# Performance work log

Measured on AMD Instinct MI355X. Metric: run time of the kernel, lower is better.

## Reference

```python
import jax, jax.numpy as jnp
import numpy as np

N = 20000      # nodes / tokens
H = 256        # hidden_size
NH = 8         # num_heads
HD = NH * H    # num_heads * hidden_size = 2048
EPS = 1e-5


def setup_inputs() -> dict:
    key = jax.random.key(0)
    ks = jax.random.split(key, 24)

    def lin_w(k, i, o):
        # xavier-ish scale for a Linear weight stored as [in, out]
        return jax.random.normal(k, (i, o), jnp.float32) * (1.0 / np.sqrt(i))

    inp = {
        'q': jax.random.normal(ks[0], (N, H), jnp.float32),
        'k': jax.random.normal(ks[1], (N, H), jnp.float32),
        'v': jax.random.normal(ks[2], (N, H), jnp.float32),
        'layer': 1,
        'Wq1': lin_w(ks[3], H, HD), 'bq1': jnp.zeros((HD,), jnp.float32),
        'Wk1': lin_w(ks[4], H, HD), 'bk1': jnp.zeros((HD,), jnp.float32),
        'Wq2': lin_w(ks[5], H, HD), 'bq2': jnp.zeros((HD,), jnp.float32),
        'Wk2': lin_w(ks[6], H, HD), 'bk2': jnp.zeros((HD,), jnp.float32),
        'Wv':  lin_w(ks[7], H, HD), 'bv':  jnp.zeros((HD,), jnp.float32),
        'ln_g': jnp.ones((HD,), jnp.float32),
        'ln_b': jnp.zeros((HD,), jnp.float32),
        'Wo': lin_w(ks[8], HD, H), 'bo': jnp.zeros((H,), jnp.float32),
        'lq1': jax.random.normal(ks[9], (H,), jnp.float32) * 0.1,
        'lk1': jax.random.normal(ks[10], (H,), jnp.float32) * 0.1,
        'lq2': jax.random.normal(ks[11], (H,), jnp.float32) * 0.1,
        'lk2': jax.random.normal(ks[12], (H,), jnp.float32) * 0.1,
    }
    return inp


def reference(q, k, v, layer, Wq1, bq1, Wk1, bk1, Wq2, bq2, Wk2, bk2,
              Wv, bv, ln_g, ln_b, Wo, bo, lq1, lk1, lq2, lk2):
    # projections: [N, H] -> [N, HD]
    q1 = q @ Wq1 + bq1
    k1 = k @ Wk1 + bk1
    q2 = q @ Wq2 + bq2
    k2 = k @ Wk2 + bk2
    vv = v @ Wv + bv

    # linear attention: K^T V -> [HD, HD]  (dropout is identity in eval mode)
    k1v = k1.T @ vv
    k2v = k2.T @ vv

    # lambda gating (scalars)
    lam1 = jnp.exp(jnp.sum(lq1 * lk1))
    lam2 = jnp.exp(jnp.sum(lq2 * lk2))
    lam_init = 0.8 - 0.6 * jnp.exp(jnp.asarray(-0.3 * layer, jnp.float32))
    lam_full = lam1 - lam2 + lam_init

    # Q @ (K^T V), differential subtraction: [N, HD]
    x = q1 @ k1v - lam_full * (q2 @ k2v)

    # LayerNorm over last dim (biased variance, eps=1e-5, like torch)
    mu = jnp.mean(x, axis=-1, keepdims=True)
    var = jnp.mean(jnp.square(x - mu), axis=-1, keepdims=True)
    x = (x - mu) / jnp.sqrt(var + EPS) * ln_g + ln_b

    x = x * (1.0 - lam_init)
    return x @ Wo + bo  # [N, H]
```

## Files before the change

### kernel.cpp

```cpp
#include <hip/hip_runtime.h>
#include <stdint.h>

typedef __bf16 bf16x8 __attribute__((ext_vector_type(8)));
typedef float f32x4 __attribute__((ext_vector_type(4)));
typedef float f32x2 __attribute__((ext_vector_type(2)));
typedef unsigned short u16x4 __attribute__((ext_vector_type(4)));
typedef unsigned short u16x8 __attribute__((ext_vector_type(8)));

#define NTOK 20000
#define HIW  256
#define HD   2048
#define LDK  66
#define BUFS 8448

static __device__ __forceinline__ unsigned short f2bf(float f) {
  union { float f; unsigned u; } c; c.f = f;
  unsigned u = c.u + (0x7fffu + ((c.u >> 16) & 1u));
  return (unsigned short)(u >> 16);
}
static __device__ __forceinline__ float bf2f(unsigned short h) {
  union { unsigned u; float f; } c; c.u = ((unsigned)h) << 16;
  return c.f;
}

#define WRED(x) { x += __shfl_xor(x,32); x += __shfl_xor(x,16); x += __shfl_xor(x,8); \
                  x += __shfl_xor(x,4);  x += __shfl_xor(x,2);  x += __shfl_xor(x,1); }

__global__ __launch_bounds__(512) void k_front(
    const float* __restrict__ kk, const float* __restrict__ vv,
    const float* __restrict__ Wq1, const float* __restrict__ Wk1,
    const float* __restrict__ Wq2, const float* __restrict__ Wk2,
    const float* __restrict__ lq1, const float* __restrict__ lk1,
    const float* __restrict__ lq2, const float* __restrict__ lk2,
    const float* __restrict__ bq1, const float* __restrict__ bk1,
    const float* __restrict__ bq2, const float* __restrict__ bk2,
    const int* __restrict__ layer,
    float* __restrict__ S_part, float* __restrict__ skp, float* __restrict__ svp,
    float* __restrict__ Pc_part, float* __restrict__ scal) {
  __shared__ unsigned short SH[4 * BUFS];
  const int b = blockIdx.x;
  const int t = threadIdx.x, lane = t & 63, wave = t >> 6;
  const int wr = (wave >> 1) * 32, wc = (wave & 1) * 64;
  const int r15 = lane & 15, kg = (lane >> 4) * 8;

  if (b < 256) {
    const int z = b & 63, by = (b >> 6) & 1, bx = (b >> 7) & 1;
    const int i0 = bx * 128, j0 = by * 128;
    const int n_lo = z * 313;
    const int cnt = (NTOK - n_lo < 313) ? (NTOK - n_lo) : 313;
    f32x4 acc[2][4];
    #pragma unroll
    for (int m = 0; m < 2; ++m)
      #pragma unroll
      for (int n = 0; n < 4; ++n) acc[m][n] = (f32x4){0.f, 0.f, 0.f, 0.f};

    const int matsel = t >> 8, col = t & 127, half = (t >> 7) & 1;
    const float* src = matsel ? vv : kk;
    const int gcol = (matsel ? j0 : i0) + col;
    unsigned short* Lb0 = SH + matsel * BUFS;
    unsigned short* Lb1 = SH + 2 * BUFS + matsel * BUFS;
    const int tbase = half * 32;
    float csum = 0.f;
    float rA[32], rB[32];

#define LOADK(dst, KT)                                                        \
    { _Pragma("unroll")                                                       \
      for (int g = 0; g < 32; ++g) {                                          \
        int nn = (KT) * 64 + tbase + g;                                       \
        dst[g] = (nn < cnt) ? src[(size_t)(n_lo + nn) * HIW + gcol] : 0.f;    \
      } }
#define WRITEK(dstp, rr)                                                      \
    { _Pragma("unroll")                                                       \
      for (int g4 = 0; g4 < 8; ++g4) {                                        \
        u16x4 o;                                                              \
        _Pragma("unroll")                                                     \
        for (int u = 0; u < 4; ++u) {                                         \
          float x = rr[g4 * 4 + u]; csum += x; o[u] = f2bf(x);                \
        }                                                                     \
        *(u16x4*)&dstp[col * LDK + tbase + g4 * 4] = o;                       \
      } }

    LOADK(rA, 0)
    WRITEK(Lb0, rA)
    LOADK(rB, 1)
    asm volatile("s_waitcnt lgkmcnt(0)" ::: "memory");
    __builtin_amdgcn_s_barrier();

    #pragma unroll
    for (int kt = 0; kt < 5; ++kt) {
      const unsigned short* Akr = SH + (kt & 1) * 2 * BUFS;
      const unsigned short* Bkr = Akr + BUFS;
      #pragma unroll
      for (int ks = 0; ks < 2; ++ks) {
        const int ko = ks * 32 + kg;
        bf16x8 ah[2], bh[4];
        #pragma unroll
        for (int m = 0; m < 2; ++m)
          ah[m] = *(const bf16x8*)&Akr[(wr + m * 16 + r15) * LDK + ko];
        #pragma unroll
        for (int n = 0; n < 4; ++n)
          bh[n] = *(const bf16x8*)&Bkr[(wc + n * 16 + r15) * LDK + ko];
        #pragma unroll
        for (int m = 0; m < 2; ++m)
          #pragma unroll
          for (int n = 0; n < 4; ++n)
            acc[m][n] = __builtin_amdgcn_mfma_f32_16x16x32_bf16(ah[m], bh[n], acc[m][n], 0, 0, 0);
      }
      if (kt < 4) {
        unsigned short* Ld = SH + ((kt + 1) & 1) * 2 * BUFS + matsel * BUFS;
        if ((kt & 1) == 0) {
          WRITEK(Ld, rB)
          if (kt + 2 <= 4) LOADK(rA, kt + 2)
        } else {
          WRITEK(Ld, rA)
          if (kt + 2 <= 4) LOADK(rB, kt + 2)
        }
      }
      asm volatile("s_waitcnt lgkmcnt(0)" ::: "memory");
      __builtin_amdgcn_s_barrier();
    }
#undef LOADK
#undef WRITEK
    const int rg = (lane >> 4) * 4;
    #pragma unroll
    for (int m = 0; m < 2; ++m)
      #pragma unroll
      for (int n = 0; n < 4; ++n)
        #pragma unroll
        for (int r = 0; r < 4; ++r)
          S_part[(size_t)z * 65536 + (i0 + wr + m * 16 + rg + r) * 256 + (j0 + wc + n * 16 + r15)] =
              acc[m][n][r];
    if (bx == by) {
      float* red = (float*)SH;
      red[t] = csum;
      __syncthreads();
      if (t < 128)      skp[z * 256 + i0 + t]         = red[t] + red[t + 128];
      else if (t < 256) svp[z * 256 + j0 + (t - 128)] = red[t + 128] + red[t + 256];
    }
  } else if (b < 384) {
    const int idx = b - 256;
    const int pair = idx >> 6, rem = idx & 63;
    const int z = rem & 15, by = (rem >> 4) & 1, bx = (rem >> 5) & 1;
    const int i0 = bx * 128, j0 = by * 128;
    const float* Wa = pair ? Wq2 : Wq1;
    const float* Wb = pair ? Wk2 : Wk1;
    f32x4 acc[2][4];
    #pragma unroll
    for (int m = 0; m < 2; ++m)
      #pragma unroll
      for (int n = 0; n < 4; ++n) acc[m][n] = (f32x4){0.f, 0.f, 0.f, 0.f};
    unsigned short* Ak = SH;
    unsigned short* Bk = SH + BUFS;
    const int srow = t >> 2, sq = (t & 3) * 16;
    for (int kt = 0; kt < 2; ++kt) {
      const int kb = z * 128 + kt * 64 + sq;
      __syncthreads();
      #pragma unroll
      for (int c = 0; c < 4; ++c) {
        f32x4 a = *(const f32x4*)&Wa[(size_t)(i0 + srow) * HD + kb + c * 4];
        f32x4 bb = *(const f32x4*)&Wb[(size_t)(j0 + srow) * HD + kb + c * 4];
        u16x4 oa, ob;
        #pragma unroll
        for (int u = 0; u < 4; ++u) { oa[u] = f2bf(a[u]); ob[u] = f2bf(bb[u]); }
        *(u16x4*)&Ak[srow * LDK + sq + c * 4] = oa;
        *(u16x4*)&Bk[srow * LDK + sq + c * 4] = ob;
      }
      __syncthreads();
      #pragma unroll
      for (int ks = 0; ks < 2; ++ks) {
        const int ko = ks * 32 + kg;
        bf16x8 ah[2], bh[4];
        #pragma unroll
        for (int m = 0; m < 2; ++m)
          ah[m] = *(const bf16x8*)&Ak[(wr + m * 16 + r15) * LDK + ko];
        #pragma unroll
        for (int n = 0; n < 4; ++n)
          bh[n] = *(const bf16x8*)&Bk[(wc + n * 16 + r15) * LDK + ko];
        #pragma unroll
        for (int m = 0; m < 2; ++m)
          #pragma unroll
          for (int n = 0; n < 4; ++n)
            acc[m][n] = __builtin_amdgcn_mfma_f32_16x16x32_bf16(ah[m], bh[n], acc[m][n], 0, 0, 0);
      }
    }
    const int rg = (lane >> 4) * 4;
    #pragma unroll
    for (int m = 0; m < 2; ++m)
      #pragma unroll
      for (int n = 0; n < 4; ++n)
        #pragma unroll
        for (int r = 0; r < 4; ++r)
          Pc_part[(size_t)(pair * 16 + z) * 65536 +
                  (i0 + wr + m * 16 + rg + r) * 256 + (j0 + wc + n * 16 + r15)] = acc[m][n][r];
  } else {
    float* red = (float*)SH;
    if (t < 256) {
      float p1 = lq1[t] * lk1[t], p2 = lq2[t] * lk2[t];
      float d1 = 0.f, d2 = 0.f;
      #pragma unroll
      for (int u = 0; u < 8; ++u) {
        d1 += bq1[t * 8 + u] * bk1[t * 8 + u];
        d2 += bq2[t * 8 + u] * bk2[t * 8 + u];
      }
      WRED(p1); WRED(p2); WRED(d1); WRED(d2);
      int w = t >> 6;
      if ((t & 63) == 0) { red[w] = p1; red[4 + w] = p2; red[8 + w] = d1; red[12 + w] = d2; }
    }
    __syncthreads();
    if (t == 0) {
      float s1 = red[0] + red[1] + red[2] + red[3];
      float s2 = red[4] + red[5] + red[6] + red[7];
      float dd1 = red[8] + red[9] + red[10] + red[11];
      float dd2 = red[12] + red[13] + red[14] + red[15];
      float li = 0.8f - 0.6f * expf(-0.3f * (float)layer[0]);
      float lam = expf(s1) - expf(s2) + li;
      scal[0] = lam; scal[1] = -lam; scal[2] = 1.0f - li; scal[3] = li;
      scal[4] = dd1 - lam * dd2;
    }
  }
}

__global__ __launch_bounds__(256) void k_sred(
    const float* __restrict__ S_part, const float* __restrict__ Pc_part,
    const float* __restrict__ skp, const float* __restrict__ svp,
    float* __restrict__ S, float* __restrict__ Pc,
    float* __restrict__ sk, float* __restrict__ sv,
    const float* __restrict__ Wk1, const float* __restrict__ Wk2,
    const float* __restrict__ Wq1, const float* __restrict__ Wq2,
    const float* __restrict__ bq1, const float* __restrict__ bq2,
    const float* __restrict__ bk1, const float* __restrict__ bk2,
    const float* __restrict__ scal, float* __restrict__ gc, float* __restrict__ uc) {
  int b = blockIdx.x, t = threadIdx.x;
  if (b < 64) {
    size_t idx = (size_t)b * 1024 + t * 4;
    f32x4 s0 = {0.f, 0.f, 0.f, 0.f}, s1 = {0.f, 0.f, 0.f, 0.f};
    #pragma unroll 4
    for (int z = 0; z < 64; z += 2) {
      s0 += *(const f32x4*)&S_part[(size_t)z * 65536 + idx];
      s1 += *(const f32x4*)&S_part[(size_t)(z + 1) * 65536 + idx];
    }
    *(f32x4*)&S[idx] = s0 + s1;
  } else if (b < 128) {
    size_t idx = (size_t)(b - 64) * 1024 + t * 4;
    f32x4 s1 = {0.f, 0.f, 0.f, 0.f}, s2 = {0.f, 0.f, 0.f, 0.f};
    #pragma unroll
    for (int z = 0; z < 16; ++z) {
      s1 += *(const f32x4*)&Pc_part[(size_t)z * 65536 + idx];
      s2 += *(const f32x4*)&Pc_part[(size_t)(16 + z) * 65536 + idx];
    }
    float lam = scal[0];
    f32x4 o;
    #pragma unroll
    for (int u = 0; u < 4; ++u) o[u] = s1[u] - lam * s2[u];
    *(f32x4*)&Pc[idx] = o;
  } else if (b < 130) {
    const float* src = (b == 128) ? skp : svp;
    float s = 0.f;
    for (int z = 0; z < 64; ++z) s += src[z * 256 + t];
    if (b == 128) sk[t] = s; else sv[t] = s;
  } else {
    int bb = b - 130, lane = t & 63, w = t >> 6;
    bool dogc = bb < 16;
    const float* A1 = dogc ? Wk1 : Wq1;
    const float* A2 = dogc ? Wk2 : Wq2;
    const float* x1 = dogc ? bq1 : bk1;
    const float* x2 = dogc ? bq2 : bk2;
    float* outv = dogc ? gc : uc;
    float lam = scal[0];
    int rb = (bb & 15) * 16 + w * 4;
    for (int q2 = 0; q2 < 4; ++q2) {
      int row = rb + q2;
      float s1 = 0.f, s2 = 0.f;
      #pragma unroll
      for (int c = 0; c < 8; ++c) {
        int kk2 = c * 256 + lane * 4;
        f32x4 a1 = *(const f32x4*)&A1[(size_t)row * HD + kk2];
        f32x4 a2 = *(const f32x4*)&A2[(size_t)row * HD + kk2];
        f32x4 v1 = *(const f32x4*)&x1[kk2];
        f32x4 v2 = *(const f32x4*)&x2[kk2];
        #pragma unroll
        for (int u = 0; u < 4; ++u) { s1 += a1[u] * v1[u]; s2 += a2[u] * v2[u]; }
      }
      WRED(s1); WRED(s2);
      if (lane == 0) outv[row] = s1 - lam * s2;
    }
  }
}

__global__ __launch_bounds__(256) void k_ac(
    const float* __restrict__ Pc, const float* __restrict__ S,
    const float* __restrict__ gc, const float* __restrict__ sk,
    float* __restrict__ Ac, float* __restrict__ tc, float* __restrict__ rv,
    float* __restrict__ scal) {
  int b = blockIdx.x, t = threadIdx.x;
  if (b < 32) {
    __shared__ float Pt[32][68];
    __shared__ float St[64][68];
    int i0 = (b >> 2) * 32, j0 = (b & 3) * 64;
    int ti = t >> 5, tj = t & 31;
    float acc[4][2] = {};
    for (int kt = 0; kt < 256; kt += 64) {
      __syncthreads();
      {
        int rr = t >> 3, c8 = (t & 7) * 8;
        *(f32x4*)&Pt[rr][c8] = *(const f32x4*)&Pc[(i0 + rr) * 256 + kt + c8];
        *(f32x4*)&Pt[rr][c8 + 4] = *(const f32x4*)&Pc[(i0 + rr) * 256 + kt + c8 + 4];
      }
      {
        int rr = t >> 2, c16 = (t & 3) * 16;
        #pragma unroll
        for (int c = 0; c < 4; ++c)
          *(f32x4*)&St[rr][c16 + c * 4] = *(const f32x4*)&S[(kt + rr) * 256 + j0 + c16 + c * 4];
      }
      __syncthreads();
      #pragma unroll 8
      for (int k2 = 0; k2 < 64; ++k2) {
        float a[4];
        #pragma unroll
        for (int u = 0; u < 4; ++u) a[u] = Pt[ti * 4 + u][k2];
        f32x2 b2 = *(const f32x2*)&St[k2][tj * 2];
        #pragma unroll
        for (int u = 0; u < 4; ++u) { acc[u][0] += a[u] * b2[0]; acc[u][1] += a[u] * b2[1]; }
      }
    }
    #pragma unroll
    for (int u = 0; u < 4; ++u) {
      Ac[(i0 + ti * 4 + u) * 256 + j0 + tj * 2] = acc[u][0];
      Ac[(i0 + ti * 4 + u) * 256 + j0 + tj * 2 + 1] = acc[u][1];
    }
  } else if (b == 32) {
    int lane = t & 63, w = t >> 6;
    f32x4 sk4 = *(const f32x4*)&sk[lane * 4];
    for (int ii = 0; ii < 64; ++ii) {
      int i = w * 64 + ii;
      f32x4 p4 = *(const f32x4*)&Pc[i * 256 + lane * 4];
      float s = p4[0] * sk4[0] + p4[1] * sk4[1] + p4[2] * sk4[2] + p4[3] * sk4[3];
      WRED(s);
      if (lane == 0) tc[i] = s;
    }
  } else {
    float s0 = 0.f, s1 = 0.f, s2 = 0.f, s3 = 0.f;
    #pragma unroll 4
    for (int i = 0; i < 256; i += 4) {
      s0 += gc[i] * S[i * 256 + t];
      s1 += gc[i + 1] * S[(i + 1) * 256 + t];
      s2 += gc[i + 2] * S[(i + 2) * 256 + t];
      s3 += gc[i + 3] * S[(i + 3) * 256 + t];
    }
    rv[t] = (s0 + s1) + (s2 + s3);
    if (t < 64) {
      f32x4 g4 = *(const f32x4*)&gc[t * 4];
      f32x4 sk4 = *(const f32x4*)&sk[t * 4];
      float a = g4[0] * sk4[0] + g4[1] * sk4[1] + g4[2] * sk4[2] + g4[3] * sk4[3];
      WRED(a);
      if (t == 0) scal[5] = a;
    }
  }
}

__global__ __launch_bounds__(256) void k_wcc_part(
    const float* __restrict__ Wv, const float* __restrict__ sv,
    const float* __restrict__ rv, float* __restrict__ part) {
  __shared__ float red[2][2][128];
  int t = threadIdx.x;
  int jblk = blockIdx.x & 15, iseg = blockIdx.x >> 4;
  int j = jblk * 128 + (t & 127);
  int half = t >> 7;
  int ib = iseg * 32 + half * 16;
  float sw = 0.f, sc = 0.f;
  #pragma unroll
  for (int u = 0; u < 16; ++u) {
    float w = Wv[(size_t)(ib + u) * HD + j];
    sw += w * sv[ib + u];
    sc += w * rv[ib + u];
  }
  red[half][0][t & 127] = sw;
  red[half][1][t & 127] = sc;
  __syncthreads();
  if (half == 0) {
    sw += red[1][0][t & 127];
    sc += red[1][1][t & 127];
    part[(iseg * 2) * 2048 + j] = sw;
    part[(iseg * 2 + 1) * 2048 + j] = sc;
  }
}

__global__ __launch_bounds__(256) void k_gc(
    const float* __restrict__ Ac, const float* __restrict__ Wv,
    const float* __restrict__ tc, const float* __restrict__ uc,
    const float* __restrict__ part, const float* __restrict__ bv,
    const float* __restrict__ scal, float* __restrict__ Gc, float* __restrict__ cc) {
  __shared__ float At[64][68];
  __shared__ float Bt[64][132];
  int t = threadIdx.x;
  int i0 = blockIdx.x * 64, j0 = blockIdx.y * 128;
  int ti = t >> 5, tj = t & 31;
  float acc[8][4] = {};
  for (int kt = 0; kt < 256; kt += 64) {
    __syncthreads();
    {
      int rr = t >> 2, c16 = (t & 3) * 16;
      #pragma unroll
      for (int c = 0; c < 4; ++c)
        *(f32x4*)&At[rr][c16 + c * 4] = *(const f32x4*)&Ac[(i0 + rr) * 256 + kt + c16 + c * 4];
    }
    {
      int rr = t >> 2, c32 = (t & 3) * 32;
      #pragma unroll
      for (int c = 0; c < 8; ++c)
        *(f32x4*)&Bt[rr][c32 + c * 4] = *(const f32x4*)&Wv[(size_t)(kt + rr) * HD + j0 + c32 + c * 4];
    }
    __syncthreads();
    #pragma unroll 8
    for (int k2 = 0; k2 < 64; ++k2) {
      float a[8];
      #pragma unroll
      for (int u = 0; u < 8; ++u) a[u] = At[ti * 8 + u][k2];
      f32x4 b = *(const f32x4*)&Bt[k2][tj * 4];
      #pragma unroll
      for (int u = 0; u < 8; ++u)
        #pragma unroll
        for (int v = 0; v < 4; ++v) acc[u][v] += a[u] * b[v];
    }
  }
  int j = j0 + tj * 4;
  f32x4 sw4 = {0.f, 0.f, 0.f, 0.f}, sc4 = {0.f, 0.f, 0.f, 0.f};
  #pragma unroll
  for (int p = 0; p < 8; ++p) {
    sw4 += *(const f32x4*)&part[(p * 2) * 2048 + j];
    sc4 += *(const f32x4*)&part[(p * 2 + 1) * 2048 + j];
  }
  f32x4 bv4 = *(const f32x4*)&bv[j];
  f32x4 wnb;
  #pragma unroll
  for (int v = 0; v < 4; ++v) wnb[v] = sw4[v] + 20000.0f * bv4[v];
  if (blockIdx.x == 0 && ti == 0) {
    float ac = scal[5], dc = scal[4];
    f32x4 ccv;
    #pragma unroll
    for (int v = 0; v < 4; ++v) ccv[v] = sc4[v] + ac * bv4[v] + dc * wnb[v];
    *(f32x4*)&cc[j] = ccv;
  }
  #pragma unroll
  for (int u = 0; u < 8; ++u) {
    int i = i0 + ti * 8 + u;
    float tci = tc[i], uci = uc[i];
    f32x4 o;
    #pragma unroll
    for (int v = 0; v < 4; ++v)
      o[v] = acc[u][v] + tci * bv4[v] + uci * wnb[v];
    *(f32x4*)&Gc[(size_t)i * HD + j] = o;
  }
}

__global__ __launch_bounds__(256) void k_post(
    const float* __restrict__ Gc, const float* __restrict__ cc,
    const float* __restrict__ Wo, const float* __restrict__ g,
    const float* __restrict__ lnb, const float* __restrict__ scal_c,
    unsigned short* __restrict__ Bbt, float* __restrict__ M_part,
    float* __restrict__ Hc_part, float* __restrict__ scal) {
  __shared__ float SMEM[6528];
  int b = blockIdx.x, t = threadIdx.x;
  if (b < 17) {
    int lane = t & 63, w = t >> 6;
    if (b < 16) {
      int rb = b * 16 + w * 4;
      for (int q2 = 0; q2 < 4; ++q2) {
        int row = rb + q2;
        float s1 = 0.f, s2 = 0.f;
        #pragma unroll
        for (int c = 0; c < 8; ++c) {
          int kk2 = c * 256 + lane * 4;
          f32x4 g4 = *(const f32x4*)&Gc[(size_t)row * HD + kk2];
          f32x4 c4v = *(const f32x4*)&cc[kk2];
          #pragma unroll
          for (int u = 0; u < 4; ++u) { s1 += g4[u]; s2 += g4[u] * c4v[u]; }
        }
        WRED(s1); WRED(s2);
        if (lane == 0) {
          Bbt[512 * 256 + row] = f2bf(s1 * (1.0f / 2048.0f));
          Bbt[513 * 256 + row] = f2bf(s2);
        }
      }
    } else {
      float s1 = 0.f, s2 = 0.f;
      #pragma unroll
      for (int c = 0; c < 2; ++c) {
        f32x4 v = *(const f32x4*)&cc[t * 8 + c * 4];
        #pragma unroll
        for (int u = 0; u < 4; ++u) { s1 += v[u]; s2 += v[u] * v[u]; }
      }
      WRED(s1); WRED(s2);
      if (lane == 0) { SMEM[w] = s1; SMEM[4 + w] = s2; }
      __syncthreads();
      if (t == 0) {
        scal[6] = SMEM[4] + SMEM[5] + SMEM[6] + SMEM[7];
        scal[7] = (SMEM[0] + SMEM[1] + SMEM[2] + SMEM[3]) * (1.0f / 2048.0f);
      }
      for (int idx = t; idx < 14 * 256; idx += 256) Bbt[514 * 256 + idx] = 0;
    }
  } else if (b < 273) {
    float (*Gi)[68] = (float(*)[68])SMEM;
    float (*Gj)[68] = (float(*)[68])(SMEM + 32 * 68);
    int idx = b - 17;
    int bx = idx & 7, by = (idx >> 3) & 7, z = idx >> 6;
    int i0 = bx * 32, j0 = by * 32;
    int ti = t >> 4, tj = t & 15;
    float acc[2][2] = {};
    for (int kt = 0; kt < 512; kt += 64) {
      int kb = z * 512 + kt;
      __syncthreads();
      {
        int rr = t >> 3, c8 = (t & 7) * 8;
        *(f32x4*)&Gi[rr][c8] = *(const f32x4*)&Gc[(size_t)(i0 + rr) * HD + kb + c8];
        *(f32x4*)&Gi[rr][c8 + 4] = *(const f32x4*)&Gc[(size_t)(i0 + rr) * HD + kb + c8 + 4];
        *(f32x4*)&Gj[rr][c8] = *(const f32x4*)&Gc[(size_t)(j0 + rr) * HD + kb + c8];
        *(f32x4*)&Gj[rr][c8 + 4] = *(const f32x4*)&Gc[(size_t)(j0 + rr) * HD + kb + c8 + 4];
      }
      __syncthreads();
      #pragma unroll 8
      for (int k2 = 0; k2 < 64; ++k2) {
        float a0 = Gi[ti * 2][k2], a1 = Gi[ti * 2 + 1][k2];
        float b0 = Gj[tj * 2][k2], b1 = Gj[tj * 2 + 1][k2];
        acc[0][0] += a0 * b0; acc[0][1] += a0 * b1;
        acc[1][0] += a1 * b0; acc[1][1] += a1 * b1;
      }
    }
    #pragma unroll
    for (int u = 0; u < 2; ++u)
      #pragma unroll
      for (int v = 0; v < 2; ++v)
        M_part[(size_t)z * 65536 + (i0 + ti * 2 + u) * 256 + j0 + tj * 2 + v] = acc[u][v];
  } else {
    float (*At)[68] = (float(*)[68])SMEM;
    float (*Bt)[68] = (float(*)[68])(SMEM + 32 * 68);
    int idx = b - 273;
    int bx = idx % 9, rem = idx / 9, by = rem & 3, z = rem >> 2;
    int i0 = bx * 32, j0 = by * 64;
    float s2 = scal_c[2];
    int ti = t >> 5, tj = t & 31;
    float acc[4][2] = {};
    for (int kt = 0; kt < 512; kt += 64) {
      int kb = z * 512 + kt;
      __syncthreads();
      {
        int rr = t >> 3, c8 = (t & 7) * 8, gi = i0 + rr;
        #pragma unroll
        for (int h = 0; h < 8; h += 4) {
          f32x4 g4 = *(const f32x4*)&g[kb + c8 + h];
          f32x4 a;
          if (gi < 256) {
            f32x4 gg = *(const f32x4*)&Gc[(size_t)gi * HD + kb + c8 + h];
            #pragma unroll
            for (int u = 0; u < 4; ++u) a[u] = gg[u] * g4[u];
          } else if (gi == 256) {
            a = g4;
          } else if (gi == 257) {
            f32x4 c4v = *(const f32x4*)&cc[kb + c8 + h];
            #pragma unroll
            for (int u = 0; u < 4; ++u) a[u] = c4v[u] * g4[u];
          } else if (gi == 258) {
            a = *(const f32x4*)&lnb[kb + c8 + h];
          } else {
            a = (f32x4){0.f, 0.f, 0.f, 0.f};
          }
          *(f32x4*)&At[rr][c8 + h] = a;
        }
      }
      {
        int rr = t >> 2, c16 = (t & 3) * 16;
        #pragma unroll
        for (int c = 0; c < 4; ++c) {
          f32x4 bb = *(const f32x4*)&Wo[(size_t)(kb + rr) * 256 + j0 + c16 + c * 4];
          #pragma unroll
          for (int u = 0; u < 4; ++u) bb[u] *= s2;
          *(f32x4*)&Bt[rr][c16 + c * 4] = bb;
        }
      }
      __syncthreads();
      #pragma unroll 8
      for (int k2 = 0; k2 < 64; ++k2) {
        float a[4];
        #pragma unroll
        for (int u = 0; u < 4; ++u) a[u] = At[ti * 4 + u][k2];
        f32x2 b2 = *(const f32x2*)&Bt[k2][tj * 2];
        #pragma unroll
        for (int u = 0; u < 4; ++u) { acc[u][0] += a[u] * b2[0]; acc[u][1] += a[u] * b2[1]; }
      }
    }
    #pragma unroll
    for (int u = 0; u < 4; ++u) {
      Hc_part[(size_t)z * 73728 + (i0 + ti * 4 + u) * 256 + j0 + tj * 2] = acc[u][0];
      Hc_part[(size_t)z * 73728 + (i0 + ti * 4 + u) * 256 + j0 + tj * 2 + 1] = acc[u][1];
    }
  }
}

__global__ __launch_bounds__(256) void k_red2(
    const float* __restrict__ M_part, const float* __restrict__ Hc_part,
    const float* __restrict__ bo, unsigned short* __restrict__ Bbt,
    float* __restrict__ wbar, float* __restrict__ hcv, float* __restrict__ bcv) {
  int bi = blockIdx.x, z2 = blockIdx.y, t = threadIdx.x;
  if (z2 == 2) {
    if (bi != 0) return;
    float s0 = 0.f, s1 = 0.f, s2 = 0.f;
    #pragma unroll
    for (int z = 0; z < 4; ++z) {
      s0 += Hc_part[(size_t)z * 73728 + 256 * 256 + t];
      s1 += Hc_part[(size_t)z * 73728 + 257 * 256 + t];
      s2 += Hc_part[(size_t)z * 73728 + 258 * 256 + t];
    }
    wbar[t] = s0; hcv[t] = s1; bcv[t] = s2 + bo[t];
    return;
  }
  __shared__ unsigned short T[64][256];
  const float* src = z2 ? Hc_part : M_part;
  const size_t sp = z2 ? 73728 : 65536;
  const int base = z2 ? 256 : 0;
  for (int ii = 0; ii < 64; ++ii) {
    int i = bi * 64 + ii;
    float s = 0.f;
    #pragma unroll
    for (int z = 0; z < 4; ++z) s += src[z * sp + i * 256 + t];
    T[ii][t] = f2bf(s);
  }
  __syncthreads();
  #pragma unroll
  for (int c = 0; c < 64; c += 8) {
    u16x8 o;
    #pragma unroll
    for (int u = 0; u < 8; ++u) o[u] = T[c + u][t];
    *(u16x8*)&Bbt[(size_t)(base + t) * 256 + bi * 64 + c] = o;
  }
}

__global__ __launch_bounds__(256) void k_out(
    const float* __restrict__ q, const unsigned short* __restrict__ Bbt,
    const float* __restrict__ hcv, const float* __restrict__ wbar,
    const float* __restrict__ bcv, const float* __restrict__ scal,
    float* __restrict__ out) {
  __shared__ unsigned short As[32 * 264];
  __shared__ float sqp[2][32];
  __shared__ float muL[32], m2L[32];
  const int t = threadIdx.x, lane = t & 63, wave = t >> 6;
  const int row0 = blockIdx.x * 32;
  const int r15 = lane & 15, kg = lane >> 4;
  {
    int r = t >> 3;
    #pragma unroll
    for (int ci = 0; ci < 8; ++ci) {
      int col = ci * 32 + (t & 7) * 4;
      f32x4 v = *(const f32x4*)&q[(size_t)(row0 + r) * HIW + col];
      u16x4 o;
      #pragma unroll
      for (int u = 0; u < 4; ++u) o[u] = f2bf(v[u]);
      *(u16x4*)&As[r * 264 + col] = o;
    }
  }
  __syncthreads();
  const int wc = wave * 128;
  f32x4 acc[2][9];
  #pragma unroll
  for (int m = 0; m < 2; ++m)
    #pragma unroll
    for (int n = 0; n < 9; ++n) acc[m][n] = (f32x4){0.f, 0.f, 0.f, 0.f};
  #pragma unroll
  for (int ko = 0; ko < 8; ++ko) {
    bf16x8 af0 = *(const bf16x8*)&As[r15 * 264 + ko * 32 + kg * 8];
    bf16x8 af1 = *(const bf16x8*)&As[(16 + r15) * 264 + ko * 32 + kg * 8];
    #pragma unroll
    for (int ni = 0; ni < 9; ++ni) {
      if (ni == 8 && wave != 3) continue;
      int colb = wc + ni * 16 + r15;
      bf16x8 bfr = *(const bf16x8*)&Bbt[(size_t)colb * 256 + ko * 32 + kg * 8];
      acc[0][ni] = __builtin_amdgcn_mfma_f32_16x16x32_bf16(af0, bfr, acc[0][ni], 0, 0, 0);
      acc[1][ni] = __builtin_amdgcn_mfma_f32_16x16x32_bf16(af1, bfr, acc[1][ni], 0, 0, 0);
    }
  }
  if (wave < 2) {
    #pragma unroll
    for (int m = 0; m < 2; ++m)
      #pragma unroll
      for (int r = 0; r < 4; ++r) {
        int rowl = m * 16 + kg * 4 + r;
        float p = 0.f;
        #pragma unroll
        for (int ni = 0; ni < 8; ++ni) {
          int col = wc + ni * 16 + r15;
          p += acc[m][ni][r] * bf2f(As[rowl * 264 + col]);
        }
        p += __shfl_xor(p, 1); p += __shfl_xor(p, 2);
        p += __shfl_xor(p, 4); p += __shfl_xor(p, 8);
        if (r15 == 0) sqp[wave][rowl] = p;
      }
  }
  if (wave == 3) {
    #pragma unroll
    for (int m = 0; m < 2; ++m)
      #pragma unroll
      for (int r = 0; r < 4; ++r) {
        int rowl = m * 16 + kg * 4 + r;
        if (r15 == 0) muL[rowl] = acc[m][8][r];
        if (r15 == 1) m2L[rowl] = acc[m][8][r];
      }
  }
  __syncthreads();
  if (wave >= 2) {
    const float css = scal[6], cbar = scal[7];
    #pragma unroll
    for (int m = 0; m < 2; ++m)
      #pragma unroll
      for (int r = 0; r < 4; ++r) {
        int rowl = m * 16 + kg * 4 + r;
        float mu = muL[rowl] + cbar;
        float ss = sqp[0][rowl] + sqp[1][rowl] + 2.0f * m2L[rowl] + css;
        float var = ss * (1.0f / 2048.0f) - mu * mu;
        float rstd = rsqrtf(var + 1e-5f);
        int grow = row0 + rowl;
        #pragma unroll
        for (int ni = 0; ni < 8; ++ni) {
          int oc = (wc - 256) + ni * 16 + r15;
          float zv = acc[m][ni][r] + hcv[oc];
          out[(size_t)grow * HIW + oc] = rstd * (zv - mu * wbar[oc]) + bcv[oc];
        }
      }
  }
}

extern "C" void kernel_launch(void* const* d_in, const int* in_sizes, int n_in,
                              void* d_out, int out_size, void* d_ws, size_t ws_size,
                              hipStream_t stream) {
  const float* q   = (const float*)d_in[0];
  const float* k   = (const float*)d_in[1];
  const float* v   = (const float*)d_in[2];
  const int* layer = (const int*)d_in[3];
  const float* Wq1 = (const float*)d_in[4];  const float* bq1 = (const float*)d_in[5];
  const float* Wk1 = (const float*)d_in[6];  const float* bk1 = (const float*)d_in[7];
  const float* Wq2 = (const float*)d_in[8];  const float* bq2 = (const float*)d_in[9];
  const float* Wk2 = (const float*)d_in[10]; const float* bk2 = (const float*)d_in[11];
  const float* Wv  = (const float*)d_in[12]; const float* bv  = (const float*)d_in[13];
  const float* lng = (const float*)d_in[14]; const float* lnb = (const float*)d_in[15];
  const float* Wo  = (const float*)d_in[16]; const float* bo  = (const float*)d_in[17];
  const float* lq1 = (const float*)d_in[18]; const float* lk1 = (const float*)d_in[19];
  const float* lq2 = (const float*)d_in[20]; const float* lk2 = (const float*)d_in[21];

  char* p = (char*)d_ws;
  float* S_part = (float*)p;  p += (size_t)64 * 65536 * 4;
  float* skp = (float*)p;     p += 64 * 256 * 4;
  float* svp = (float*)p;     p += 64 * 256 * 4;
  float* Pc_part = (float*)p; p += (size_t)32 * 65536 * 4;
  float* S  = (float*)p;      p += 65536 * 4;
  float* Pc = (float*)p;      p += 65536 * 4;
  float* sk = (float*)p;      p += 1024;
  float* sv = (float*)p;      p += 1024;
  float* gc = (float*)p;      p += 1024;
  float* uc = (float*)p;      p += 1024;
  float* tc = (float*)p;      p += 1024;
  float* rv = (float*)p;      p += 1024;
  float* wcc_part = (float*)p; p += (size_t)16 * 2048 * 4;
  float* cc  = (float*)p;     p += 2048 * 4;
  float* Ac  = (float*)p;     p += 65536 * 4;
  float* Gc  = (float*)p;     p += (size_t)2048 * 256 * 4;
  float* M_part  = (float*)p; p += (size_t)4 * 65536 * 4;
  float* Hc_part = (float*)p; p += (size_t)4 * 288 * 256 * 4;
  unsigned short* Bbt = (unsigned short*)p; p += (size_t)528 * 256 * 2;
  float* wbar = (float*)p;    p += 1024;
  float* hcv  = (float*)p;    p += 1024;
  float* bcv  = (float*)p;    p += 1024;
  float* scal = (float*)p;    p += 256;

  const dim3 b256(256);
  k_front<<<dim3(385), dim3(512), 0, stream>>>(k, v, Wq1, Wk1, Wq2, Wk2,
      lq1, lk1, lq2, lk2, bq1, bk1, bq2, bk2, layer, S_part, skp, svp, Pc_part, scal);
  k_sred<<<dim3(162), b256, 0, stream>>>(S_part, Pc_part, skp, svp, S, Pc, sk, sv,
                                         Wk1, Wk2, Wq1, Wq2, bq1, bq2, bk1, bk2, scal, gc, uc);
  k_ac<<<dim3(34), b256, 0, stream>>>(Pc, S, gc, sk, Ac, tc, rv, scal);
  k_wcc_part<<<dim3(128), b256, 0, stream>>>(Wv, sv, rv, wcc_part);
  k_gc<<<dim3(4, 16), b256, 0, stream>>>(Ac, Wv, tc, uc, wcc_part, bv, scal, Gc, cc);
  k_post<<<dim3(417), b256, 0, stream>>>(Gc, cc, Wo, lng, lnb, scal, Bbt, M_part, Hc_part, scal);
  k_red2<<<dim3(4, 3), b256, 0, stream>>>(M_part, Hc_part, bo, Bbt, wbar, hcv, bcv);
  k_out<<<dim3(625), b256, 0, stream>>>(q, Bbt, hcv, wbar, bcv, scal, (float*)d_out);
}
```

Measured before the change: 179.1 us.

## Store partials in bf16, fuse wcc into k_gc, retile Gram, pre-swizzle Bt

Split-K partial sums for S and Pc are now written and read as bf16 instead of fp32, halving the reduction traffic in k_front/k_sred. The separate k_wcc_part kernel is folded into k_gc's inner loop, which removes one launch. The k_post Gram block uses larger 64x64 tiles with 8x2 register blocking, so fewer blocks are launched. The Bt operand is stored in an MFMA-fragment-swizzled layout so k_out reads it contiguously. Conversions use the native __bf16 cast, and s_setprio is wrapped around the MFMA loops. Rounding the partials to bf16 adds accumulation error.

```diff
diff --git a/kernel.cpp b/kernel.cpp
--- a/kernel.cpp
+++ b/kernel.cpp
@@ -2,6 +2,7 @@
 #include <stdint.h>
 
 typedef __bf16 bf16x8 __attribute__((ext_vector_type(8)));
+typedef __bf16 bf16x4v __attribute__((ext_vector_type(4)));
 typedef float f32x4 __attribute__((ext_vector_type(4)));
 typedef float f32x2 __attribute__((ext_vector_type(2)));
 typedef unsigned short u16x4 __attribute__((ext_vector_type(4)));
@@ -13,18 +14,18 @@
 #define LDK  66
 #define BUFS 8448
 
-static __device__ __forceinline__ unsigned short f2bf(float f) {
-  union { float f; unsigned u; } c; c.f = f;
-  unsigned u = c.u + (0x7fffu + ((c.u >> 16) & 1u));
-  return (unsigned short)(u >> 16);
-}
 static __device__ __forceinline__ float bf2f(unsigned short h) {
   union { unsigned u; float f; } c; c.u = ((unsigned)h) << 16;
   return c.f;
 }
+static __device__ __forceinline__ unsigned short fbits(float x) {
+  __bf16 h = (__bf16)x;
+  return __builtin_bit_cast(unsigned short, h);
+}
 
 #define WRED(x) { x += __shfl_xor(x,32); x += __shfl_xor(x,16); x += __shfl_xor(x,8); \
                   x += __shfl_xor(x,4);  x += __shfl_xor(x,2);  x += __shfl_xor(x,1); }
+
 
 __global__ __launch_bounds__(512) void k_front(
     const float* __restrict__ kk, const float* __restrict__ vv,
@@ -35,8 +36,8 @@
     const float* __restrict__ bq1, const float* __restrict__ bk1,
     const float* __restrict__ bq2, const float* __restrict__ bk2,
     const int* __restrict__ layer,
-    float* __restrict__ S_part, float* __restrict__ skp, float* __restrict__ svp,
-    float* __restrict__ Pc_part, float* __restrict__ scal) {
+    unsigned short* __restrict__ S_part, float* __restrict__ skp, float* __restrict__ svp,
+    unsigned short* __restrict__ Pc_part, float* __restrict__ scal) {
   __shared__ unsigned short SH[4 * BUFS];
   const int b = blockIdx.x;
   const int t = threadIdx.x, lane = t & 63, wave = t >> 6;
@@ -58,7 +59,6 @@
     const float* src = matsel ? vv : kk;
     const int gcol = (matsel ? j0 : i0) + col;
     unsigned short* Lb0 = SH + matsel * BUFS;
-    unsigned short* Lb1 = SH + 2 * BUFS + matsel * BUFS;
     const int tbase = half * 32;
     float csum = 0.f;
     float rA[32], rB[32];
@@ -72,12 +72,12 @@
 #define WRITEK(dstp, rr)                                                      \
     { _Pragma("unroll")                                                       \
       for (int g4 = 0; g4 < 8; ++g4) {                                        \
-        u16x4 o;                                                              \
+        bf16x4v o;                                                            \
         _Pragma("unroll")                                                     \
         for (int u = 0; u < 4; ++u) {                                         \
-          float x = rr[g4 * 4 + u]; csum += x; o[u] = f2bf(x);                \
+          float x = rr[g4 * 4 + u]; csum += x; o[u] = (__bf16)x;              \
         }                                                                     \
-        *(u16x4*)&dstp[col * LDK + tbase + g4 * 4] = o;                       \
+        *(bf16x4v*)&dstp[col * LDK + tbase + g4 * 4] = o;                     \
       } }
 
     LOADK(rA, 0)
@@ -90,6 +90,7 @@
     for (int kt = 0; kt < 5; ++kt) {
       const unsigned short* Akr = SH + (kt & 1) * 2 * BUFS;
       const unsigned short* Bkr = Akr + BUFS;
+      __builtin_amdgcn_s_setprio(1);
       #pragma unroll
       for (int ks = 0; ks < 2; ++ks) {
         const int ko = ks * 32 + kg;
@@ -106,6 +107,7 @@
           for (int n = 0; n < 4; ++n)
             acc[m][n] = __builtin_amdgcn_mfma_f32_16x16x32_bf16(ah[m], bh[n], acc[m][n], 0, 0, 0);
       }
+      __builtin_amdgcn_s_setprio(0);
       if (kt < 4) {
         unsigned short* Ld = SH + ((kt + 1) & 1) * 2 * BUFS + matsel * BUFS;
         if ((kt & 1) == 0) {
@@ -122,14 +124,14 @@
 #undef LOADK
 #undef WRITEK
     const int rg = (lane >> 4) * 4;
+    unsigned short* Sp = S_part + (size_t)z * 65536;
     #pragma unroll
     for (int m = 0; m < 2; ++m)
       #pragma unroll
       for (int n = 0; n < 4; ++n)
         #pragma unroll
         for (int r = 0; r < 4; ++r)
-          S_part[(size_t)z * 65536 + (i0 + wr + m * 16 + rg + r) * 256 + (j0 + wc + n * 16 + r15)] =
-              acc[m][n][r];
+          Sp[(i0 + wr + m * 16 + rg + r) * 256 + (j0 + wc + n * 16 + r15)] = fbits(acc[m][n][r]);
     if (bx == by) {
       float* red = (float*)SH;
       red[t] = csum;
@@ -159,13 +161,14 @@
       for (int c = 0; c < 4; ++c) {
         f32x4 a = *(const f32x4*)&Wa[(size_t)(i0 + srow) * HD + kb + c * 4];
         f32x4 bb = *(const f32x4*)&Wb[(size_t)(j0 + srow) * HD + kb + c * 4];
-        u16x4 oa, ob;
-        #pragma unroll
-        for (int u = 0; u < 4; ++u) { oa[u] = f2bf(a[u]); ob[u] = f2bf(bb[u]); }
-        *(u16x4*)&Ak[srow * LDK + sq + c * 4] = oa;
-        *(u16x4*)&Bk[srow * LDK + sq + c * 4] = ob;
-      }
-      __syncthreads();
+        bf16x4v oa, ob;
+        #pragma unroll
+        for (int u = 0; u < 4; ++u) { oa[u] = (__bf16)a[u]; ob[u] = (__bf16)bb[u]; }
+        *(bf16x4v*)&Ak[srow * LDK + sq + c * 4] = oa;
+        *(bf16x4v*)&Bk[srow * LDK + sq + c * 4] = ob;
+      }
+      __syncthreads();
+      __builtin_amdgcn_s_setprio(1);
       #pragma unroll
       for (int ks = 0; ks < 2; ++ks) {
         const int ko = ks * 32 + kg;
@@ -182,16 +185,17 @@
           for (int n = 0; n < 4; ++n)
             acc[m][n] = __builtin_amdgcn_mfma_f32_16x16x32_bf16(ah[m], bh[n], acc[m][n], 0, 0, 0);
       }
+      __builtin_amdgcn_s_setprio(0);
     }
     const int rg = (lane >> 4) * 4;
+    unsigned short* Pp = Pc_part + (size_t)(pair * 16 + z) * 65536;
     #pragma unroll
     for (int m = 0; m < 2; ++m)
       #pragma unroll
       for (int n = 0; n < 4; ++n)
         #pragma unroll
         for (int r = 0; r < 4; ++r)
-          Pc_part[(size_t)(pair * 16 + z) * 65536 +
-                  (i0 + wr + m * 16 + rg + r) * 256 + (j0 + wc + n * 16 + r15)] = acc[m][n][r];
+          Pp[(i0 + wr + m * 16 + rg + r) * 256 + (j0 + wc + n * 16 + r15)] = fbits(acc[m][n][r]);
   } else {
     float* red = (float*)SH;
     if (t < 256) {
@@ -221,7 +225,7 @@
 }
 
 __global__ __launch_bounds__(256) void k_sred(
-    const float* __restrict__ S_part, const float* __restrict__ Pc_part,
+    const unsigned short* __restrict__ S_part, const unsigned short* __restrict__ Pc_part,
     const float* __restrict__ skp, const float* __restrict__ svp,
     float* __restrict__ S, float* __restrict__ Pc,
     float* __restrict__ sk, float* __restrict__ sv,
@@ -233,33 +237,34 @@
   int b = blockIdx.x, t = threadIdx.x;
   if (b < 64) {
     size_t idx = (size_t)b * 1024 + t * 4;
-    f32x4 s0 = {0.f, 0.f, 0.f, 0.f}, s1 = {0.f, 0.f, 0.f, 0.f};
+    f32x4 s = {0.f, 0.f, 0.f, 0.f};
     #pragma unroll 4
-    for (int z = 0; z < 64; z += 2) {
-      s0 += *(const f32x4*)&S_part[(size_t)z * 65536 + idx];
-      s1 += *(const f32x4*)&S_part[(size_t)(z + 1) * 65536 + idx];
-    }
-    *(f32x4*)&S[idx] = s0 + s1;
-  } else if (b < 128) {
-    size_t idx = (size_t)(b - 64) * 1024 + t * 4;
-    f32x4 s1 = {0.f, 0.f, 0.f, 0.f}, s2 = {0.f, 0.f, 0.f, 0.f};
-    #pragma unroll
+    for (int z = 0; z < 64; ++z) {
+      u16x4 h = *(const u16x4*)&S_part[(size_t)z * 65536 + idx];
+      #pragma unroll
+      for (int u = 0; u < 4; ++u) s[u] += bf2f(h[u]);
+    }
+    *(f32x4*)&S[idx] = s;
+  } else if (b < 96) {
+    size_t idx = (size_t)(b - 64) * 2048 + t * 8;
+    float s1[8] = {}, s2[8] = {};
+    #pragma unroll 2
     for (int z = 0; z < 16; ++z) {
-      s1 += *(const f32x4*)&Pc_part[(size_t)z * 65536 + idx];
-      s2 += *(const f32x4*)&Pc_part[(size_t)(16 + z) * 65536 + idx];
+      u16x8 ha = *(const u16x8*)&Pc_part[(size_t)z * 65536 + idx];
+      u16x8 hb = *(const u16x8*)&Pc_part[(size_t)(16 + z) * 65536 + idx];
+      #pragma unroll
+      for (int u = 0; u < 8; ++u) { s1[u] += bf2f(ha[u]); s2[u] += bf2f(hb[u]); }
     }
     float lam = scal[0];
-    f32x4 o;
-    #pragma unroll
-    for (int u = 0; u < 4; ++u) o[u] = s1[u] - lam * s2[u];
-    *(f32x4*)&Pc[idx] = o;
-  } else if (b < 130) {
-    const float* src = (b == 128) ? skp : svp;
+    #pragma unroll
+    for (int u = 0; u < 8; ++u) Pc[idx + u] = s1[u] - lam * s2[u];
+  } else if (b < 98) {
+    const float* src = (b == 96) ? skp : svp;
     float s = 0.f;
     for (int z = 0; z < 64; ++z) s += src[z * 256 + t];
-    if (b == 128) sk[t] = s; else sv[t] = s;
+    if (b == 96) sk[t] = s; else sv[t] = s;
   } else {
-    int bb = b - 130, lane = t & 63, w = t >> 6;
+    int bb = b - 98, lane = t & 63, w = t >> 6;
     bool dogc = bb < 16;
     const float* A1 = dogc ? Wk1 : Wq1;
     const float* A2 = dogc ? Wk2 : Wq2;
@@ -358,44 +363,21 @@
   }
 }
 
-__global__ __launch_bounds__(256) void k_wcc_part(
-    const float* __restrict__ Wv, const float* __restrict__ sv,
-    const float* __restrict__ rv, float* __restrict__ part) {
-  __shared__ float red[2][2][128];
-  int t = threadIdx.x;
-  int jblk = blockIdx.x & 15, iseg = blockIdx.x >> 4;
-  int j = jblk * 128 + (t & 127);
-  int half = t >> 7;
-  int ib = iseg * 32 + half * 16;
-  float sw = 0.f, sc = 0.f;
-  #pragma unroll
-  for (int u = 0; u < 16; ++u) {
-    float w = Wv[(size_t)(ib + u) * HD + j];
-    sw += w * sv[ib + u];
-    sc += w * rv[ib + u];
-  }
-  red[half][0][t & 127] = sw;
-  red[half][1][t & 127] = sc;
-  __syncthreads();
-  if (half == 0) {
-    sw += red[1][0][t & 127];
-    sc += red[1][1][t & 127];
-    part[(iseg * 2) * 2048 + j] = sw;
-    part[(iseg * 2 + 1) * 2048 + j] = sc;
-  }
-}
-
 __global__ __launch_bounds__(256) void k_gc(
     const float* __restrict__ Ac, const float* __restrict__ Wv,
     const float* __restrict__ tc, const float* __restrict__ uc,
-    const float* __restrict__ part, const float* __restrict__ bv,
-    const float* __restrict__ scal, float* __restrict__ Gc, float* __restrict__ cc) {
+    const float* __restrict__ sv, const float* __restrict__ rv,
+    const float* __restrict__ bv, const float* __restrict__ scal,
+    float* __restrict__ Gc, float* __restrict__ cc) {
   __shared__ float At[64][68];
   __shared__ float Bt[64][132];
+  __shared__ float svr[256], rvr[256];
   int t = threadIdx.x;
   int i0 = blockIdx.x * 64, j0 = blockIdx.y * 128;
   int ti = t >> 5, tj = t & 31;
+  svr[t] = sv[t]; rvr[t] = rv[t];
   float acc[8][4] = {};
+  f32x4 swa = {0.f, 0.f, 0.f, 0.f}, sca = {0.f, 0.f, 0.f, 0.f};
   for (int kt = 0; kt < 256; kt += 64) {
     __syncthreads();
     {
@@ -417,6 +399,8 @@
       #pragma unroll
       for (int u = 0; u < 8; ++u) a[u] = At[ti * 8 + u][k2];
       f32x4 b = *(const f32x4*)&Bt[k2][tj * 4];
+      float svk = svr[kt + k2], rvk = rvr[kt + k2];
+      swa += b * svk; sca += b * rvk;
       #pragma unroll
       for (int u = 0; u < 8; ++u)
         #pragma unroll
@@ -424,21 +408,15 @@
     }
   }
   int j = j0 + tj * 4;
-  f32x4 sw4 = {0.f, 0.f, 0.f, 0.f}, sc4 = {0.f, 0.f, 0.f, 0.f};
-  #pragma unroll
-  for (int p = 0; p < 8; ++p) {
-    sw4 += *(const f32x4*)&part[(p * 2) * 2048 + j];
-    sc4 += *(const f32x4*)&part[(p * 2 + 1) * 2048 + j];
-  }
   f32x4 bv4 = *(const f32x4*)&bv[j];
   f32x4 wnb;
   #pragma unroll
-  for (int v = 0; v < 4; ++v) wnb[v] = sw4[v] + 20000.0f * bv4[v];
+  for (int v = 0; v < 4; ++v) wnb[v] = swa[v] + 20000.0f * bv4[v];
   if (blockIdx.x == 0 && ti == 0) {
     float ac = scal[5], dc = scal[4];
     f32x4 ccv;
     #pragma unroll
-    for (int v = 0; v < 4; ++v) ccv[v] = sc4[v] + ac * bv4[v] + dc * wnb[v];
+    for (int v = 0; v < 4; ++v) ccv[v] = sca[v] + ac * bv4[v] + dc * wnb[v];
     *(f32x4*)&cc[j] = ccv;
   }
   #pragma unroll
@@ -457,9 +435,9 @@
     const float* __restrict__ Gc, const float* __restrict__ cc,
     const float* __restrict__ Wo, const float* __restrict__ g,
     const float* __restrict__ lnb, const float* __restrict__ scal_c,
-    unsigned short* __restrict__ Bbt, float* __restrict__ M_part,
+    unsigned short* __restrict__ Bt2, float* __restrict__ M_part,
     float* __restrict__ Hc_part, float* __restrict__ scal) {
-  __shared__ float SMEM[6528];
+  __shared__ float SMEM[8768];
   int b = blockIdx.x, t = threadIdx.x;
   if (b < 17) {
     int lane = t & 63, w = t >> 6;
@@ -478,8 +456,9 @@
         }
         WRED(s1); WRED(s2);
         if (lane == 0) {
-          Bbt[512 * 256 + row] = f2bf(s1 * (1.0f / 2048.0f));
-          Bbt[513 * 256 + row] = f2bf(s2);
+          int base = ((256 + (row >> 5)) * 64 + ((row >> 3) & 3) * 16) * 8 + (row & 7);
+          Bt2[base] = fbits(s1 * (1.0f / 2048.0f));
+          Bt2[base + 8] = fbits(s2);
         }
       }
     } else {
@@ -491,50 +470,57 @@
         for (int u = 0; u < 4; ++u) { s1 += v[u]; s2 += v[u] * v[u]; }
       }
       WRED(s1); WRED(s2);
-      if (lane == 0) { SMEM[w] = s1; SMEM[4 + w] = s2; }
+      if ((t & 63) == 0) { SMEM[t >> 6] = s1; SMEM[4 + (t >> 6)] = s2; }
       __syncthreads();
       if (t == 0) {
         scal[6] = SMEM[4] + SMEM[5] + SMEM[6] + SMEM[7];
         scal[7] = (SMEM[0] + SMEM[1] + SMEM[2] + SMEM[3]) * (1.0f / 2048.0f);
       }
-      for (int idx = t; idx < 14 * 256; idx += 256) Bbt[514 * 256 + idx] = 0;
-    }
-  } else if (b < 273) {
+      for (int idx = t; idx < 14 * 256; idx += 256) {
+        int ci = idx >> 8, kk2 = idx & 255;
+        int col = 514 + ci;
+        Bt2[((256 + (kk2 >> 5)) * 64 + ((kk2 >> 3) & 3) * 16 + (col & 15)) * 8 + (kk2 & 7)] = 0;
+      }
+    }
+  } else if (b < 81) {
     float (*Gi)[68] = (float(*)[68])SMEM;
-    float (*Gj)[68] = (float(*)[68])(SMEM + 32 * 68);
+    float (*Gj)[69] = (float(*)[69])(SMEM + 64 * 68);
     int idx = b - 17;
-    int bx = idx & 7, by = (idx >> 3) & 7, z = idx >> 6;
-    int i0 = bx * 32, j0 = by * 32;
-    int ti = t >> 4, tj = t & 15;
-    float acc[2][2] = {};
+    int bx = idx & 3, by = (idx >> 2) & 3, z = idx >> 4;
+    int i0 = bx * 64, j0 = by * 64;
+    int ti = t >> 5, tj = t & 31;
+    float acc[8][2] = {};
     for (int kt = 0; kt < 512; kt += 64) {
       int kb = z * 512 + kt;
       __syncthreads();
       {
-        int rr = t >> 3, c8 = (t & 7) * 8;
-        *(f32x4*)&Gi[rr][c8] = *(const f32x4*)&Gc[(size_t)(i0 + rr) * HD + kb + c8];
-        *(f32x4*)&Gi[rr][c8 + 4] = *(const f32x4*)&Gc[(size_t)(i0 + rr) * HD + kb + c8 + 4];
-        *(f32x4*)&Gj[rr][c8] = *(const f32x4*)&Gc[(size_t)(j0 + rr) * HD + kb + c8];
-        *(f32x4*)&Gj[rr][c8 + 4] = *(const f32x4*)&Gc[(size_t)(j0 + rr) * HD + kb + c8 + 4];
+        int rr = t >> 2, c16 = (t & 3) * 16;
+        #pragma unroll
+        for (int c = 0; c < 4; ++c) {
+          *(f32x4*)&Gi[rr][c16 + c * 4] = *(const f32x4*)&Gc[(size_t)(i0 + rr) * HD + kb + c16 + c * 4];
+          *(f32x4*)&Gj[rr][c16 + c * 4] = *(const f32x4*)&Gc[(size_t)(j0 + rr) * HD + kb + c16 + c * 4];
+        }
       }
       __syncthreads();
       #pragma unroll 8
       for (int k2 = 0; k2 < 64; ++k2) {
-        float a0 = Gi[ti * 2][k2], a1 = Gi[ti * 2 + 1][k2];
+        float a[8];
+        #pragma unroll
+        for (int u = 0; u < 8; ++u) a[u] = Gi[ti * 8 + u][k2];
         float b0 = Gj[tj * 2][k2], b1 = Gj[tj * 2 + 1][k2];
-        acc[0][0] += a0 * b0; acc[0][1] += a0 * b1;
-        acc[1][0] += a1 * b0; acc[1][1] += a1 * b1;
-      }
-    }
-    #pragma unroll
-    for (int u = 0; u < 2; ++u)
-      #pragma unroll
-      for (int v = 0; v < 2; ++v)
-        M_part[(size_t)z * 65536 + (i0 + ti * 2 + u) * 256 + j0 + tj * 2 + v] = acc[u][v];
+        #pragma unroll
+        for (int u = 0; u < 8; ++u) { acc[u][0] += a[u] * b0; acc[u][1] += a[u] * b1; }
+      }
+    }
+    #pragma unroll
+    for (int u = 0; u < 8; ++u) {
+      M_part[(size_t)z * 65536 + (i0 + ti * 8 + u) * 256 + j0 + tj * 2] = acc[u][0];
+      M_part[(size_t)z * 65536 + (i0 + ti * 8 + u) * 256 + j0 + tj * 2 + 1] = acc[u][1];
+    }
   } else {
     float (*At)[68] = (float(*)[68])SMEM;
     float (*Bt)[68] = (float(*)[68])(SMEM + 32 * 68);
-    int idx = b - 273;
+    int idx = b - 81;
     int bx = idx % 9, rem = idx / 9, by = rem & 3, z = rem >> 2;
     int i0 = bx * 32, j0 = by * 64;
     float s2 = scal_c[2];
@@ -598,7 +584,7 @@
 
 __global__ __launch_bounds__(256) void k_red2(
     const float* __restrict__ M_part, const float* __restrict__ Hc_part,
-    const float* __restrict__ bo, unsigned short* __restrict__ Bbt,
+    const float* __restrict__ bo, unsigned short* __restrict__ Bt2,
     float* __restrict__ wbar, float* __restrict__ hcv, float* __restrict__ bcv) {
   int bi = blockIdx.x, z2 = blockIdx.y, t = threadIdx.x;
   if (z2 == 2) {
@@ -622,20 +608,23 @@
     float s = 0.f;
     #pragma unroll
     for (int z = 0; z < 4; ++z) s += src[z * sp + i * 256 + t];
-    T[ii][t] = f2bf(s);
+    T[ii][t] = fbits(s);
   }
   __syncthreads();
+  const int col = base + t;
   #pragma unroll
   for (int c = 0; c < 64; c += 8) {
     u16x8 o;
     #pragma unroll
     for (int u = 0; u < 8; ++u) o[u] = T[c + u][t];
-    *(u16x8*)&Bbt[(size_t)(base + t) * 256 + bi * 64 + c] = o;
+    int kk0 = bi * 64 + c;
+    int addr = (((col >> 4) * 8 + (kk0 >> 5)) * 64 + ((kk0 >> 3) & 3) * 16 + (col & 15)) * 8;
+    *(u16x8*)&Bt2[addr] = o;
   }
 }
 
 __global__ __launch_bounds__(256) void k_out(
-    const float* __restrict__ q, const unsigned short* __restrict__ Bbt,
+    const float* __restrict__ q, const unsigned short* __restrict__ Bt2,
     const float* __restrict__ hcv, const float* __restrict__ wbar,
     const float* __restrict__ bcv, const float* __restrict__ scal,
     float* __restrict__ out) {
@@ -651,19 +640,21 @@
     for (int ci = 0; ci < 8; ++ci) {
       int col = ci * 32 + (t & 7) * 4;
       f32x4 v = *(const f32x4*)&q[(size_t)(row0 + r) * HIW + col];
-      u16x4 o;
-      #pragma unroll
-      for (int u = 0; u < 4; ++u) o[u] = f2bf(v[u]);
-      *(u16x4*)&As[r * 264 + col] = o;
+      bf16x4v o;
+      #pragma unroll
+      for (int u = 0; u < 4; ++u) o[u] = (__bf16)v[u];
+      *(bf16x4v*)&As[r * 264 + col] = o;
     }
   }
   __syncthreads();
   const int wc = wave * 128;
+  const unsigned short* bbase = Bt2 + (size_t)(wave * 8) * 4096 + (size_t)lane * 8;
   f32x4 acc[2][9];
   #pragma unroll
   for (int m = 0; m < 2; ++m)
     #pragma unroll
     for (int n = 0; n < 9; ++n) acc[m][n] = (f32x4){0.f, 0.f, 0.f, 0.f};
+  __builtin_amdgcn_s_setprio(1);
   #pragma unroll
   for (int ko = 0; ko < 8; ++ko) {
     bf16x8 af0 = *(const bf16x8*)&As[r15 * 264 + ko * 32 + kg * 8];
@@ -671,12 +662,12 @@
     #pragma unroll
     for (int ni = 0; ni < 9; ++ni) {
       if (ni == 8 && wave != 3) continue;
-      int colb = wc + ni * 16 + r15;
-      bf16x8 bfr = *(const bf16x8*)&Bbt[(size_t)colb * 256 + ko * 32 + kg * 8];
+      bf16x8 bfr = *(const bf16x8*)&bbase[ni * 4096 + ko * 512];
       acc[0][ni] = __builtin_amdgcn_mfma_f32_16x16x32_bf16(af0, bfr, acc[0][ni], 0, 0, 0);
       acc[1][ni] = __builtin_amdgcn_mfma_f32_16x16x32_bf16(af1, bfr, acc[1][ni], 0, 0, 0);
     }
   }
+  __builtin_amdgcn_s_setprio(0);
   if (wave < 2) {
     #pragma unroll
     for (int m = 0; m < 2; ++m)
@@ -745,10 +736,10 @@
   const float* lq2 = (const float*)d_in[20]; const float* lk2 = (const float*)d_in[21];
 
   char* p = (char*)d_ws;
-  float* S_part = (float*)p;  p += (size_t)64 * 65536 * 4;
+  unsigned short* S_part = (unsigned short*)p;  p += (size_t)64 * 65536 * 2;
   float* skp = (float*)p;     p += 64 * 256 * 4;
   float* svp = (float*)p;     p += 64 * 256 * 4;
-  float* Pc_part = (float*)p; p += (size_t)32 * 65536 * 4;
+  unsigned short* Pc_part = (unsigned short*)p; p += (size_t)32 * 65536 * 2;
   float* S  = (float*)p;      p += 65536 * 4;
   float* Pc = (float*)p;      p += 65536 * 4;
   float* sk = (float*)p;      p += 1024;
@@ -757,13 +748,12 @@
   float* uc = (float*)p;      p += 1024;
   float* tc = (float*)p;      p += 1024;
   float* rv = (float*)p;      p += 1024;
-  float* wcc_part = (float*)p; p += (size_t)16 * 2048 * 4;
   float* cc  = (float*)p;     p += 2048 * 4;
   float* Ac  = (float*)p;     p += 65536 * 4;
   float* Gc  = (float*)p;     p += (size_t)2048 * 256 * 4;
   float* M_part  = (float*)p; p += (size_t)4 * 65536 * 4;
   float* Hc_part = (float*)p; p += (size_t)4 * 288 * 256 * 4;
-  unsigned short* Bbt = (unsigned short*)p; p += (size_t)528 * 256 * 2;
+  unsigned short* Bt2 = (unsigned short*)p; p += (size_t)135168 * 2;
   float* wbar = (float*)p;    p += 1024;
   float* hcv  = (float*)p;    p += 1024;
   float* bcv  = (float*)p;    p += 1024;
@@ -772,12 +762,11 @@
   const dim3 b256(256);
   k_front<<<dim3(385), dim3(512), 0, stream>>>(k, v, Wq1, Wk1, Wq2, Wk2,
       lq1, lk1, lq2, lk2, bq1, bk1, bq2, bk2, layer, S_part, skp, svp, Pc_part, scal);
-  k_sred<<<dim3(162), b256, 0, stream>>>(S_part, Pc_part, skp, svp, S, Pc, sk, sv,
+  k_sred<<<dim3(130), b256, 0, stream>>>(S_part, Pc_part, skp, svp, S, Pc, sk, sv,
                                          Wk1, Wk2, Wq1, Wq2, bq1, bq2, bk1, bk2, scal, gc, uc);
   k_ac<<<dim3(34), b256, 0, stream>>>(Pc, S, gc, sk, Ac, tc, rv, scal);
-  k_wcc_part<<<dim3(128), b256, 0, stream>>>(Wv, sv, rv, wcc_part);
-  k_gc<<<dim3(4, 16), b256, 0, stream>>>(Ac, Wv, tc, uc, wcc_part, bv, scal, Gc, cc);
-  k_post<<<dim3(417), b256, 0, stream>>>(Gc, cc, Wo, lng, lnb, scal, Bbt, M_part, Hc_part, scal);
-  k_red2<<<dim3(4, 3), b256, 0, stream>>>(M_part, Hc_part, bo, Bbt, wbar, hcv, bcv);
-  k_out<<<dim3(625), b256, 0, stream>>>(q, Bbt, hcv, wbar, bcv, scal, (float*)d_out);
-}
+  k_gc<<<dim3(4, 16), b256, 0, stream>>>(Ac, Wv, tc, uc, sv, rv, bv, scal, Gc, cc);
+  k_post<<<dim3(225), b256, 0, stream>>>(Gc, cc, Wo, lng, lnb, scal, Bt2, M_part, Hc_part, scal);
+  k_red2<<<dim3(4, 3), b256, 0, stream>>>(M_part, Hc_part, bo, Bt2, wbar, hcv, bcv);
+  k_out<<<dim3(625), b256, 0, stream>>>(q, Bt2, hcv, wbar, bcv, scal, (float*)d_out);
+}
```

Result: slower. 184.5 us (+3.1%).
